# Kernel tuning notes

Hardware: AMD Instinct MI355X
Metric: run time of the kernel (lower is better)

The kernel has to match this reference:

```python
import jax, jax.numpy as jnp
import numpy as np

N = 100000   # entities
T = 4        # edge types
E = 250000   # edges per type
D = 64       # dimension
H = 4        # attention heads
C = 64       # per-head out channels (PyG out_channels)
F_IN = 256   # raw feature dim
L = 2        # num_layers
NEG_SLOPE = 0.2


def setup_inputs() -> dict:
    key = jax.random.key(0)
    ks = jax.random.split(key, 10)
    return {
        "feature_matrix": jax.random.normal(ks[0], (N, F_IN), jnp.float32),
        "entity_emb": jax.random.normal(ks[1], (N + 1, D), jnp.float32),
        "lin_w": jax.random.normal(ks[2], (F_IN, D), jnp.float32) * 0.05,
        "lin_b": jnp.zeros((D,), jnp.float32),
        "ln_g": jnp.ones((D,), jnp.float32),
        "ln_b": jnp.zeros((D,), jnp.float32),
        "W_src": jax.random.normal(ks[3], (L, T, D, H * C), jnp.float32) * 0.1,
        "W_dst": jax.random.normal(ks[4], (L, T, D, H * C), jnp.float32) * 0.1,
        "a_src": jax.random.normal(ks[5], (L, T, H, C), jnp.float32) * 0.1,
        "a_dst": jax.random.normal(ks[6], (L, T, H, C), jnp.float32) * 0.1,
        "conv_bias": jnp.zeros((L, T, C), jnp.float32),
        "edge_index": jax.random.randint(ks[7], (T, 2, E), 0, N, jnp.int32),
    }


def _layer_norm(x, g, b):
    mu = jnp.mean(x, axis=-1, keepdims=True)
    var = jnp.var(x, axis=-1, keepdims=True)
    return (x - mu) * jax.lax.rsqrt(var + 1e-5) * g + b


def _l2_normalize(x):
    n = jnp.linalg.norm(x, axis=-1, keepdims=True)
    return x / jnp.maximum(n, 1e-12)


def _gat_conv(x, src, dst, Ws, Wd, a_s, a_d, bias):
    # x: [N, D]; src/dst: [E'] (self loops already appended, PyG default)
    xs = (x @ Ws).reshape(N, H, C)          # source projection per head
    xd = (x @ Wd).reshape(N, H, C)          # destination projection per head
    logit = (xs * a_s).sum(-1)[src] + (xd * a_d).sum(-1)[dst]  # [E', H]
    logit = jax.nn.leaky_relu(logit, NEG_SLOPE)
    # segment softmax over incoming edges of each dst node
    m = jax.lax.stop_gradient(jax.ops.segment_max(logit, dst, num_segments=N))
    p = jnp.exp(logit - m[dst])
    s = jax.ops.segment_sum(p, dst, num_segments=N)
    alpha = p / s[dst]                       # [E', H]
    msg = xs[src] * alpha[..., None]         # [E', H, C]
    out = jax.ops.segment_sum(msg.reshape(-1, H * C), dst, num_segments=N)
    out = out.reshape(N, H, C).mean(axis=1)  # concat=False -> head mean
    return out + bias


def reference(feature_matrix, entity_emb, lin_w, lin_b, ln_g, ln_b,
              W_src, W_dst, a_src, a_dst, conv_bias, edge_index):
    # feature_transform: Linear -> LayerNorm -> GELU (exact erf GELU, torch default)
    xf = jax.nn.gelu(_layer_norm(feature_matrix @ lin_w + lin_b, ln_g, ln_b),
                     approximate=False)
    xe = _l2_normalize(entity_emb[:N])
    x = xf + xe
    loop = jnp.arange(N, dtype=edge_index.dtype)
    for l in range(L):
        acc = jnp.zeros((N, C), x.dtype)
        for t in range(T):
            src = jnp.concatenate([edge_index[t, 0], loop])
            dst = jnp.concatenate([edge_index[t, 1], loop])
            acc = acc + _gat_conv(x, src, dst, W_src[l, t], W_dst[l, t],
                                  a_src[l, t], a_dst[l, t], conv_bias[l, t])
        x = jax.nn.gelu(acc / T, approximate=False)  # HeteroConv aggr='mean'; dropout=eval identity
    return x
```

## Files before the change

kernel.cpp:

```cpp
#include <hip/hip_runtime.h>
#include <hip/hip_bf16.h>
#include <cstdint>

#define NN   100000
#define TT   4
#define EE   250000
#define LL   2
#define NCH  49
#define EPN  (EE + NN)
#define N64  ((size_t)NN * 64)

typedef unsigned short ushort_t;
typedef __attribute__((ext_vector_type(8))) short bf16x8;
typedef __attribute__((ext_vector_type(16))) float floatx16;

static __device__ __forceinline__ float gelu_exact(float v) {
    return 0.5f * v * (1.0f + erff(v * 0.7071067811865476f));
}
static __device__ __forceinline__ float wave_sum64(float v) {
    #pragma unroll
    for (int m = 32; m; m >>= 1) v += __shfl_xor(v, m, 64);
    return v;
}
static __device__ __forceinline__ ushort_t f2bf(float f) {
    unsigned u = __float_as_uint(f);
    u += 0x7FFFu + ((u >> 16) & 1u);
    return (ushort_t)(u >> 16);
}
static __device__ __forceinline__ float bf2f(ushort_t h) {
    return __uint_as_float((unsigned)h << 16);
}

__global__ __launch_bounds__(256) void k_prep(
    const float* __restrict__ Wsrc, const float* __restrict__ Wdst,
    const float* __restrict__ asrc, const float* __restrict__ adst,
    const float* __restrict__ cb, const float* __restrict__ lin_w,
    ushort_t* __restrict__ wcTh, ushort_t* __restrict__ wcTl,
    ushort_t* __restrict__ lwTh, ushort_t* __restrict__ lwTl,
    ushort_t* __restrict__ bpTh, ushort_t* __restrict__ bpTl,
    float* __restrict__ bsum)
{
    int id = blockIdx.x * 256 + threadIdx.x;
    {
        int d = id & 63;
        int c = (id >> 6) & 63;
        int h = (id >> 12) & 3;
        int t = (id >> 14) & 3;
        int l = (id >> 16) & 1;
        float v = 0.25f * Wsrc[(((l * 4 + t) * 64 + d) * 256) + h * 64 + c];
        int dst = (l * 64 + c) * 1024 + (t * 256 + h * 64 + d);
        ushort_t hh = f2bf(v);
        bpTh[dst] = hh;
        bpTl[dst] = f2bf(v - bf2f(hh));
    }
    if (id < LL * 64 * 64) {
        int d   = id & 63;
        int col = (id >> 6) & 63;
        int l   = (id >> 12) & 1;
        int t = col >> 3, side = (col >> 2) & 1, h = col & 3;
        const float* W = side ? Wdst : Wsrc;
        const float* a = side ? adst : asrc;
        int wb = ((l * 4 + t) * 64 + d) * 256 + h * 64;
        int ab = ((l * 4 + t) * 4 + h) * 64;
        float s = 0.f;
        #pragma unroll 8
        for (int c2 = 0; c2 < 64; ++c2) s = fmaf(W[wb + c2], a[ab + c2], s);
        int dst = (l * 64 + col) * 64 + d;
        ushort_t hh = f2bf(s);
        wcTh[dst] = hh;
        wcTl[dst] = f2bf(s - bf2f(hh));
    }
    if (id < 64 * 256) {
        int k = id & 255, c = id >> 8;
        float v = lin_w[k * 64 + c];
        ushort_t hh = f2bf(v);
        lwTh[c * 256 + k] = hh;
        lwTl[c * 256 + k] = f2bf(v - bf2f(hh));
    }
    if (id < LL * 64) {
        int l = id >> 6, c = id & 63;
        float s = 0.f;
        for (int t = 0; t < TT; ++t) s += cb[(l * 4 + t) * 64 + c];
        bsum[id] = s;
    }
}

__global__ void k_hist(const int* __restrict__ ei, int* __restrict__ cursor) {
    int id = blockIdx.x * 256 + threadIdx.x;
    if (id >= TT * EE) return;
    int t = id / EE, e = id - t * EE;
    int d = ei[(t * 2 + 1) * EE + e];
    atomicAdd(&cursor[t * NN + d], 1);
}

__global__ __launch_bounds__(256) void k_scan1(const int* __restrict__ deg,
                                               int* __restrict__ csum) {
    int b = blockIdx.x, t = b / NCH, cc = b - t * NCH;
    int tid = threadIdx.x;
    int base = cc * 2048 + tid * 8;
    int s = 0;
    #pragma unroll
    for (int i = 0; i < 8; ++i) {
        int idx = base + i;
        if (idx < NN) s += deg[t * NN + idx] + 1;
    }
    #pragma unroll
    for (int m = 32; m; m >>= 1) s += __shfl_xor(s, m, 64);
    __shared__ int ws4[4];
    int lane = tid & 63, wid = tid >> 6;
    if (lane == 0) ws4[wid] = s;
    __syncthreads();
    if (tid == 0) csum[b] = ws4[0] + ws4[1] + ws4[2] + ws4[3];
}

__global__ void k_scan2(const int* __restrict__ csum, int* __restrict__ cbase,
                        int* __restrict__ row_ptr) {
    int t = threadIdx.x;
    if (t >= TT) return;
    int base = 0;
    for (int c = 0; c < NCH; ++c) {
        cbase[t * NCH + c] = base;
        base += csum[t * NCH + c];
    }
    row_ptr[t * (NN + 1) + NN] = base;
}

__global__ __launch_bounds__(256) void k_scan3(int* __restrict__ cursor,
                                               const int* __restrict__ cbase,
                                               int* __restrict__ row_ptr) {
    int b = blockIdx.x, t = b / NCH, cc = b - t * NCH;
    int tid = threadIdx.x, lane = tid & 63, wid = tid >> 6;
    int base = cc * 2048 + tid * 8;
    int vals[8], ts = 0;
    #pragma unroll
    for (int i = 0; i < 8; ++i) {
        int idx = base + i;
        int v = (idx < NN) ? cursor[t * NN + idx] + 1 : 0;
        vals[i] = v; ts += v;
    }
    int v = ts;
    #pragma unroll
    for (int off = 1; off < 64; off <<= 1) {
        int u = __shfl_up(v, off, 64);
        if (lane >= off) v += u;
    }
    __shared__ int wt[4];
    if (lane == 63) wt[wid] = v;
    __syncthreads();
    int wbase = 0;
    for (int w = 0; w < wid; ++w) wbase += wt[w];
    int run = cbase[t * NCH + cc] + wbase + (v - ts);
    #pragma unroll
    for (int i = 0; i < 8; ++i) {
        int idx = base + i;
        if (idx < NN) {
            row_ptr[t * (NN + 1) + idx] = run;
            cursor[t * NN + idx] = run;
        }
        run += vals[i];
    }
}

__global__ void k_scatter(const int* __restrict__ ei, int* __restrict__ cursor,
                          int* __restrict__ col) {
    int id = blockIdx.x * 256 + threadIdx.x;
    if (id >= TT * EPN) return;
    int t = id / EPN, r = id - t * EPN;
    int s, d;
    if (r < EE) { s = ei[t * 2 * EE + r]; d = ei[(t * 2 + 1) * EE + r]; }
    else        { s = d = r - EE; }
    int pos = atomicAdd(&cursor[t * NN + d], 1);
    col[(size_t)t * EPN + pos] = s;
}

__global__ void k_split(const float* __restrict__ in, ushort_t* __restrict__ hi,
                        ushort_t* __restrict__ lo, int n4) {
    int i = blockIdx.x * 256 + threadIdx.x;
    if (i >= n4) return;
    float4 v = ((const float4*)in)[i];
    ushort_t h0 = f2bf(v.x), h1 = f2bf(v.y), h2 = f2bf(v.z), h3 = f2bf(v.w);
    ushort4 hv = make_ushort4(h0, h1, h2, h3);
    ushort4 lv = make_ushort4(f2bf(v.x - bf2f(h0)), f2bf(v.y - bf2f(h1)),
                              f2bf(v.z - bf2f(h2)), f2bf(v.w - bf2f(h3)));
    ((ushort4*)hi)[i] = hv;
    ((ushort4*)lo)[i] = lv;
}

template <int FLAGS>
__global__ __launch_bounds__(256, 4) void k_gemm_mx(
    const ushort_t* __restrict__ Ahi, const ushort_t* __restrict__ Alo,
    const ushort_t* __restrict__ Bhi, const ushort_t* __restrict__ Blo,
    int K, int ldb, int nrows,
    const float* __restrict__ accbuf, const float* __restrict__ bias,
    float* __restrict__ Cout, ushort_t* __restrict__ Chi, ushort_t* __restrict__ Clo)
{
    constexpr int KC = 32, LK = 40;
    __shared__ ushort_t sAh[128 * LK], sAl[128 * LK];
    __shared__ ushort_t sBh[64 * LK],  sBl[64 * LK];
    const int tid = threadIdx.x;
    const int w = tid >> 6, ln = tid & 63;
    const int l31 = ln & 31, hl = ln >> 5;
    const int rowbase = blockIdx.x * 128;

    floatx16 accv[2];
    #pragma unroll
    for (int ct = 0; ct < 2; ++ct)
        #pragma unroll
        for (int r = 0; r < 16; ++r) accv[ct][r] = 0.f;

    for (int kc = 0; kc < K; kc += KC) {
        __syncthreads();
        #pragma unroll
        for (int i = 0; i < 2; ++i) {
            int f = tid + i * 256;
            int r = f >> 2, cg = f & 3;
            int row = rowbase + r;
            int so = r * LK + cg * 8;
            if (row < nrows) {
                size_t ga = (size_t)row * K + kc + cg * 8;
                *(uint4*)&sAh[so] = *(const uint4*)(Ahi + ga);
                *(uint4*)&sAl[so] = *(const uint4*)(Alo + ga);
            } else {
                *(uint4*)&sAh[so] = make_uint4(0, 0, 0, 0);
                *(uint4*)&sAl[so] = make_uint4(0, 0, 0, 0);
            }
        }
        {
            int r = tid >> 2, cg = tid & 3;
            size_t gb = (size_t)r * ldb + kc + cg * 8;
            int so = r * LK + cg * 8;
            *(uint4*)&sBh[so] = *(const uint4*)(Bhi + gb);
            *(uint4*)&sBl[so] = *(const uint4*)(Blo + gb);
        }
        __syncthreads();
        const int arow = (w << 5) + l31;
        #pragma unroll
        for (int s = 0; s < 2; ++s) {
            const int koff = (s << 4) + (hl << 3);
            bf16x8 ah  = *(const bf16x8*)&sAh[arow * LK + koff];
            bf16x8 al  = *(const bf16x8*)&sAl[arow * LK + koff];
            bf16x8 bh0 = *(const bf16x8*)&sBh[l31 * LK + koff];
            bf16x8 bl0 = *(const bf16x8*)&sBl[l31 * LK + koff];
            bf16x8 bh1 = *(const bf16x8*)&sBh[(32 + l31) * LK + koff];
            bf16x8 bl1 = *(const bf16x8*)&sBl[(32 + l31) * LK + koff];
            accv[0] = __builtin_amdgcn_mfma_f32_32x32x16_bf16(ah, bh0, accv[0], 0, 0, 0);
            accv[1] = __builtin_amdgcn_mfma_f32_32x32x16_bf16(ah, bh1, accv[1], 0, 0, 0);
            accv[0] = __builtin_amdgcn_mfma_f32_32x32x16_bf16(al, bh0, accv[0], 0, 0, 0);
            accv[1] = __builtin_amdgcn_mfma_f32_32x32x16_bf16(al, bh1, accv[1], 0, 0, 0);
            accv[0] = __builtin_amdgcn_mfma_f32_32x32x16_bf16(ah, bl0, accv[0], 0, 0, 0);
            accv[1] = __builtin_amdgcn_mfma_f32_32x32x16_bf16(ah, bl1, accv[1], 0, 0, 0);
        }
    }
    #pragma unroll
    for (int ct = 0; ct < 2; ++ct) {
        int col = (ct << 5) + l31;
        float bv = (FLAGS & 2) ? bias[col] : 0.f;
        #pragma unroll
        for (int r = 0; r < 16; ++r) {
            int row = rowbase + (w << 5) + (r & 3) + ((r >> 2) << 3) + (hl << 2);
            if (row < nrows) {
                size_t idx = (size_t)row * 64 + col;
                float v = accv[ct][r];
                if (FLAGS & 1) v += accbuf[idx];
                if (FLAGS & 2) v = gelu_exact((v + bv) * 0.25f);
                Cout[idx] = v;
                if (FLAGS & 4) {
                    ushort_t hh = f2bf(v);
                    Chi[idx] = hh;
                    Clo[idx] = f2bf(v - bf2f(hh));
                }
            }
        }
    }
}

__global__ __launch_bounds__(256) void k_feat_post(
    const float* __restrict__ y, const float* __restrict__ lin_b,
    const float* __restrict__ ln_g, const float* __restrict__ ln_b,
    const float* __restrict__ emb, float* __restrict__ xout,
    ushort_t* __restrict__ xh, ushort_t* __restrict__ xl)
{
    int n = (blockIdx.x << 2) + (threadIdx.x >> 6);
    int c = threadIdx.x & 63;
    size_t base = (size_t)n * 64 + c;
    float v = y[base] + lin_b[c];
    float mean = wave_sum64(v) * 0.015625f;
    float t = v - mean;
    float var = wave_sum64(t * t) * 0.015625f;
    float vn = t * (1.0f / sqrtf(var + 1e-5f)) * ln_g[c] + ln_b[c];
    float g = gelu_exact(vn);
    float e = emb[base];
    float nrm = sqrtf(wave_sum64(e * e));
    float xv = g + e / fmaxf(nrm, 1e-12f);
    xout[base] = xv;
    ushort_t hh = f2bf(xv);
    xh[base] = hh;
    xl[base] = f2bf(xv - bf2f(hh));
}

__global__ __launch_bounds__(256) void k_edge2(
    const float* __restrict__ x, const float* __restrict__ s_all,
    const int* __restrict__ row_ptr, const int* __restrict__ col,
    ushort_t* __restrict__ zh, ushort_t* __restrict__ zl, int t0, int nt)
{
    int n = (blockIdx.x << 2) + (threadIdx.x >> 6);
    int lane = threadIdx.x & 63;
    int zrow = nt * 256;
    for (int tt = 0; tt < nt; ++tt) {
        int t = t0 + tt;
        int rp0 = row_ptr[t * (NN + 1) + n];
        int rp1 = row_ptr[t * (NN + 1) + n + 1];
        const int* colt = col + (size_t)t * EPN;
        const float4 sd = *(const float4*)&s_all[(size_t)n * 64 + t * 8 + 4];
        float z0 = 0.f, z1 = 0.f, z2 = 0.f, z3 = 0.f;
        float S0 = 0.f, S1 = 0.f, S2 = 0.f, S3 = 0.f;
        #pragma unroll 2
        for (int e = rp0; e < rp1; ++e) {
            int s = colt[e];
            const float4 ss = *(const float4*)&s_all[(size_t)s * 64 + t * 8];
            float l0 = ss.x + sd.x, l1 = ss.y + sd.y;
            float l2 = ss.z + sd.z, l3 = ss.w + sd.w;
            l0 = l0 > 0.f ? l0 : 0.2f * l0;
            l1 = l1 > 0.f ? l1 : 0.2f * l1;
            l2 = l2 > 0.f ? l2 : 0.2f * l2;
            l3 = l3 > 0.f ? l3 : 0.2f * l3;
            float p0 = __expf(l0), p1 = __expf(l1);
            float p2 = __expf(l2), p3 = __expf(l3);
            S0 += p0; S1 += p1; S2 += p2; S3 += p3;
            float xv = x[(size_t)s * 64 + lane];
            z0 = fmaf(p0, xv, z0);
            z1 = fmaf(p1, xv, z1);
            z2 = fmaf(p2, xv, z2);
            z3 = fmaf(p3, xv, z3);
        }
        size_t zb = (size_t)n * zrow + tt * 256 + lane;
        float v0 = z0 / S0, v1 = z1 / S1, v2 = z2 / S2, v3 = z3 / S3;
        ushort_t h0 = f2bf(v0), h1 = f2bf(v1), h2 = f2bf(v2), h3 = f2bf(v3);
        zh[zb]       = h0;  zl[zb]       = f2bf(v0 - bf2f(h0));
        zh[zb + 64]  = h1;  zl[zb + 64]  = f2bf(v1 - bf2f(h1));
        zh[zb + 128] = h2;  zl[zb + 128] = f2bf(v2 - bf2f(h2));
        zh[zb + 192] = h3;  zl[zb + 192] = f2bf(v3 - bf2f(h3));
    }
}

extern "C" void kernel_launch(void* const* d_in, const int* in_sizes, int n_in,
                              void* d_out, int out_size, void* d_ws, size_t ws_size,
                              hipStream_t stream) {
    const float* fm    = (const float*)d_in[0];
    const float* emb   = (const float*)d_in[1];
    const float* lin_w = (const float*)d_in[2];
    const float* lin_b = (const float*)d_in[3];
    const float* ln_g  = (const float*)d_in[4];
    const float* ln_b  = (const float*)d_in[5];
    const float* Wsrc  = (const float*)d_in[6];
    const float* Wdst  = (const float*)d_in[7];
    const float* asrc  = (const float*)d_in[8];
    const float* adst  = (const float*)d_in[9];
    const float* cbias = (const float*)d_in[10];
    const int*   ei    = (const int*)d_in[11];
    float* out = (float*)d_out;
    (void)in_sizes; (void)n_in; (void)out_size;

    char* w = (char*)d_ws;
    size_t off = 0;
    auto alloc = [&](size_t bytes) -> void* {
        void* p = w + off;
        off += (bytes + 255) & ~(size_t)255;
        return p;
    };
    ushort_t* wcTh = (ushort_t*)alloc((size_t)LL * 64 * 64 * 2);
    ushort_t* wcTl = (ushort_t*)alloc((size_t)LL * 64 * 64 * 2);
    ushort_t* lwTh = (ushort_t*)alloc((size_t)64 * 256 * 2);
    ushort_t* lwTl = (ushort_t*)alloc((size_t)64 * 256 * 2);
    ushort_t* bpTh = (ushort_t*)alloc((size_t)LL * 64 * 1024 * 2);
    ushort_t* bpTl = (ushort_t*)alloc((size_t)LL * 64 * 1024 * 2);
    float* bsum    = (float*)alloc((size_t)LL * 64 * 4);
    int*   row_ptr = (int*)  alloc((size_t)TT * (NN + 1) * 4);
    int*   cursor  = (int*)  alloc((size_t)TT * NN * 4);
    int*   colarr  = (int*)  alloc((size_t)TT * EPN * 4);
    int*   csum    = (int*)  alloc((size_t)TT * NCH * 4);
    int*   cbase   = (int*)  alloc((size_t)TT * NCH * 4);
    float* x       = (float*)alloc(N64 * 4);
    ushort_t* xh   = (ushort_t*)alloc(N64 * 2);
    ushort_t* xl   = (ushort_t*)alloc(N64 * 2);
    float* s_all   = (float*)alloc(N64 * 4);
    float* accB    = (float*)alloc(N64 * 4);
    size_t rem = (ws_size > off) ? (ws_size - off) : 0;
    int NT = 1;
    if (rem >= (size_t)NN * 1024 * 4 + (8u << 20)) NT = 4;
    else if (rem >= (size_t)NN * 512 * 4 + (8u << 20)) NT = 2;
    size_t planeE = (size_t)NN * 256 * NT;
    char* big = (char*)alloc(2 * planeE * 2 < 2 * (size_t)NN * 256 * 2
                             ? 2 * (size_t)NN * 256 * 2 : 2 * planeE * 2);
    ushort_t* fmh = (ushort_t*)big;
    ushort_t* fml = fmh + (size_t)NN * 256;
    ushort_t* zh  = (ushort_t*)big;
    ushort_t* zl  = zh + planeE;

    hipMemsetAsync(cursor, 0, (size_t)TT * NN * 4, stream);
    k_prep<<<512, 256, 0, stream>>>(Wsrc, Wdst, asrc, adst, cbias, lin_w,
                                    wcTh, wcTl, lwTh, lwTl, bpTh, bpTl, bsum);
    k_hist<<<(TT * EE + 255) / 256, 256, 0, stream>>>(ei, cursor);
    k_scan1<<<TT * NCH, 256, 0, stream>>>(cursor, csum);
    k_scan2<<<1, 64, 0, stream>>>(csum, cbase, row_ptr);
    k_scan3<<<TT * NCH, 256, 0, stream>>>(cursor, cbase, row_ptr);
    k_scatter<<<(TT * EPN + 255) / 256, 256, 0, stream>>>(ei, cursor, colarr);

    const int GB = (NN + 127) / 128;
    k_split<<<(NN * 64 + 255) / 256, 256, 0, stream>>>(fm, fmh, fml, NN * 64);
    k_gemm_mx<0><<<GB, 256, 0, stream>>>(fmh, fml, lwTh, lwTl, 256, 256, NN,
                                         nullptr, nullptr, accB, nullptr, nullptr);
    k_feat_post<<<NN / 4, 256, 0, stream>>>(accB, lin_b, ln_g, ln_b, emb, x, xh, xl);

    const int nb = TT / NT;
    for (int l = 0; l < LL; ++l) {
        k_gemm_mx<0><<<GB, 256, 0, stream>>>(xh, xl, wcTh + l * 4096, wcTl + l * 4096,
                                             64, 64, NN, nullptr, nullptr,
                                             s_all, nullptr, nullptr);
        float* dest = (l == 0) ? x : out;
        const ushort_t* Bh = bpTh + (size_t)l * 65536;
        const ushort_t* Bl = bpTl + (size_t)l * 65536;
        for (int b = 0; b < nb; ++b) {
            k_edge2<<<NN / 4, 256, 0, stream>>>(x, s_all, row_ptr, colarr,
                                                zh, zl, b * NT, NT);
            int K = NT * 256;
            const ushort_t* Bhb = Bh + b * K;
            const ushort_t* Blb = Bl + b * K;
            bool last = (b == nb - 1);
            if (!last) {
                if (b == 0)
                    k_gemm_mx<0><<<GB, 256, 0, stream>>>(zh, zl, Bhb, Blb, K, 1024, NN,
                                                         nullptr, nullptr, accB,
                                                         nullptr, nullptr);
                else
                    k_gemm_mx<1><<<GB, 256, 0, stream>>>(zh, zl, Bhb, Blb, K, 1024, NN,
                                                         accB, nullptr, accB,
                                                         nullptr, nullptr);
            } else {
                if (nb == 1) {
                    if (l == 0)
                        k_gemm_mx<6><<<GB, 256, 0, stream>>>(zh, zl, Bhb, Blb, K, 1024,
                                                             NN, nullptr, bsum + l * 64,
                                                             dest, xh, xl);
                    else
                        k_gemm_mx<2><<<GB, 256, 0, stream>>>(zh, zl, Bhb, Blb, K, 1024,
                                                             NN, nullptr, bsum + l * 64,
                                                             dest, nullptr, nullptr);
                } else {
                    if (l == 0)
                        k_gemm_mx<7><<<GB, 256, 0, stream>>>(zh, zl, Bhb, Blb, K, 1024,
                                                             NN, accB, bsum + l * 64,
                                                             dest, xh, xl);
                    else
                        k_gemm_mx<3><<<GB, 256, 0, stream>>>(zh, zl, Bhb, Blb, K, 1024,
                                                             NN, accB, bsum + l * 64,
                                                             dest, nullptr, nullptr);
                }
            }
        }
    }
}
```

Measured before the change: 1.057 ms.

## Fuse bf16 split into GEMM loads and precompute per-edge attention weights

The GEMM gains a mode that loads fp32 A tiles and splits them into bf16 hi/lo pairs in registers. This removes the separate k_split pass and the hi/lo copies of x written by feat_post and the layer-0 epilogue. Attention exponentials are now computed once per edge in a new k_edgep kernel, with coalesced edge-parallel reads, and stored in a buffer that k_edge2 reads. That takes the leaky-relu and exp work off the gather loop, at the cost of extra memory traffic for a per-edge dst array and a 4-float-per-edge weight buffer.

```diff
diff --git a/kernel.cpp b/kernel.cpp
--- a/kernel.cpp
+++ b/kernel.cpp
@@ -162,7 +162,7 @@
 }
 
 __global__ void k_scatter(const int* __restrict__ ei, int* __restrict__ cursor,
-                          int* __restrict__ col) {
+                          int* __restrict__ col, int* __restrict__ dstarr) {
     int id = blockIdx.x * 256 + threadIdx.x;
     if (id >= TT * EPN) return;
     int t = id / EPN, r = id - t * EPN;
@@ -171,19 +171,7 @@
     else        { s = d = r - EE; }
     int pos = atomicAdd(&cursor[t * NN + d], 1);
     col[(size_t)t * EPN + pos] = s;
-}
-
-__global__ void k_split(const float* __restrict__ in, ushort_t* __restrict__ hi,
-                        ushort_t* __restrict__ lo, int n4) {
-    int i = blockIdx.x * 256 + threadIdx.x;
-    if (i >= n4) return;
-    float4 v = ((const float4*)in)[i];
-    ushort_t h0 = f2bf(v.x), h1 = f2bf(v.y), h2 = f2bf(v.z), h3 = f2bf(v.w);
-    ushort4 hv = make_ushort4(h0, h1, h2, h3);
-    ushort4 lv = make_ushort4(f2bf(v.x - bf2f(h0)), f2bf(v.y - bf2f(h1)),
-                              f2bf(v.z - bf2f(h2)), f2bf(v.w - bf2f(h3)));
-    ((ushort4*)hi)[i] = hv;
-    ((ushort4*)lo)[i] = lv;
+    dstarr[(size_t)t * EPN + pos] = d;
 }
 
 template <int FLAGS>
@@ -218,8 +206,28 @@
             int so = r * LK + cg * 8;
             if (row < nrows) {
                 size_t ga = (size_t)row * K + kc + cg * 8;
-                *(uint4*)&sAh[so] = *(const uint4*)(Ahi + ga);
-                *(uint4*)&sAl[so] = *(const uint4*)(Alo + ga);
+                if constexpr (FLAGS & 8) {
+                    const float* Af = (const float*)Ahi;
+                    float4 v0 = *(const float4*)(Af + ga);
+                    float4 v1 = *(const float4*)(Af + ga + 4);
+                    float vf[8] = {v0.x, v0.y, v0.z, v0.w, v1.x, v1.y, v1.z, v1.w};
+                    unsigned hu[8], lu[8];
+                    #pragma unroll
+                    for (int q = 0; q < 8; ++q) {
+                        ushort_t hh = f2bf(vf[q]);
+                        hu[q] = hh;
+                        lu[q] = f2bf(vf[q] - bf2f(hh));
+                    }
+                    uint4 H = make_uint4(hu[0] | (hu[1] << 16), hu[2] | (hu[3] << 16),
+                                         hu[4] | (hu[5] << 16), hu[6] | (hu[7] << 16));
+                    uint4 L = make_uint4(lu[0] | (lu[1] << 16), lu[2] | (lu[3] << 16),
+                                         lu[4] | (lu[5] << 16), lu[6] | (lu[7] << 16));
+                    *(uint4*)&sAh[so] = H;
+                    *(uint4*)&sAl[so] = L;
+                } else {
+                    *(uint4*)&sAh[so] = *(const uint4*)(Ahi + ga);
+                    *(uint4*)&sAl[so] = *(const uint4*)(Alo + ga);
+                }
             } else {
                 *(uint4*)&sAh[so] = make_uint4(0, 0, 0, 0);
                 *(uint4*)&sAl[so] = make_uint4(0, 0, 0, 0);
@@ -277,8 +285,7 @@
 __global__ __launch_bounds__(256) void k_feat_post(
     const float* __restrict__ y, const float* __restrict__ lin_b,
     const float* __restrict__ ln_g, const float* __restrict__ ln_b,
-    const float* __restrict__ emb, float* __restrict__ xout,
-    ushort_t* __restrict__ xh, ushort_t* __restrict__ xl)
+    const float* __restrict__ emb, float* __restrict__ xout)
 {
     int n = (blockIdx.x << 2) + (threadIdx.x >> 6);
     int c = threadIdx.x & 63;
@@ -293,13 +300,31 @@
     float nrm = sqrtf(wave_sum64(e * e));
     float xv = g + e / fmaxf(nrm, 1e-12f);
     xout[base] = xv;
-    ushort_t hh = f2bf(xv);
-    xh[base] = hh;
-    xl[base] = f2bf(xv - bf2f(hh));
+}
+
+__global__ __launch_bounds__(256) void k_edgep(
+    const float* __restrict__ s_all, const int* __restrict__ col,
+    const int* __restrict__ dstarr, float* __restrict__ parr)
+{
+    int i = blockIdx.x * 256 + threadIdx.x;
+    int t = blockIdx.y;
+    if (i >= EPN) return;
+    size_t base = (size_t)t * EPN + i;
+    int s = col[base], d = dstarr[base];
+    const float4 a = *(const float4*)&s_all[(size_t)s * 64 + t * 8];
+    const float4 b = *(const float4*)&s_all[(size_t)d * 64 + t * 8 + 4];
+    float l0 = a.x + b.x, l1 = a.y + b.y;
+    float l2 = a.z + b.z, l3 = a.w + b.w;
+    l0 = l0 > 0.f ? l0 : 0.2f * l0;
+    l1 = l1 > 0.f ? l1 : 0.2f * l1;
+    l2 = l2 > 0.f ? l2 : 0.2f * l2;
+    l3 = l3 > 0.f ? l3 : 0.2f * l3;
+    float4 p = make_float4(__expf(l0), __expf(l1), __expf(l2), __expf(l3));
+    *(float4*)&parr[base * 4] = p;
 }
 
 __global__ __launch_bounds__(256) void k_edge2(
-    const float* __restrict__ x, const float* __restrict__ s_all,
+    const float* __restrict__ x, const float* __restrict__ parr,
     const int* __restrict__ row_ptr, const int* __restrict__ col,
     ushort_t* __restrict__ zh, ushort_t* __restrict__ zl, int t0, int nt)
 {
@@ -311,27 +336,19 @@
         int rp0 = row_ptr[t * (NN + 1) + n];
         int rp1 = row_ptr[t * (NN + 1) + n + 1];
         const int* colt = col + (size_t)t * EPN;
-        const float4 sd = *(const float4*)&s_all[(size_t)n * 64 + t * 8 + 4];
+        const float4* pt = (const float4*)parr + (size_t)t * EPN;
         float z0 = 0.f, z1 = 0.f, z2 = 0.f, z3 = 0.f;
         float S0 = 0.f, S1 = 0.f, S2 = 0.f, S3 = 0.f;
         #pragma unroll 2
         for (int e = rp0; e < rp1; ++e) {
             int s = colt[e];
-            const float4 ss = *(const float4*)&s_all[(size_t)s * 64 + t * 8];
-            float l0 = ss.x + sd.x, l1 = ss.y + sd.y;
-            float l2 = ss.z + sd.z, l3 = ss.w + sd.w;
-            l0 = l0 > 0.f ? l0 : 0.2f * l0;
-            l1 = l1 > 0.f ? l1 : 0.2f * l1;
-            l2 = l2 > 0.f ? l2 : 0.2f * l2;
-            l3 = l3 > 0.f ? l3 : 0.2f * l3;
-            float p0 = __expf(l0), p1 = __expf(l1);
-            float p2 = __expf(l2), p3 = __expf(l3);
-            S0 += p0; S1 += p1; S2 += p2; S3 += p3;
+            float4 p = pt[e];
             float xv = x[(size_t)s * 64 + lane];
-            z0 = fmaf(p0, xv, z0);
-            z1 = fmaf(p1, xv, z1);
-            z2 = fmaf(p2, xv, z2);
-            z3 = fmaf(p3, xv, z3);
+            S0 += p.x; S1 += p.y; S2 += p.z; S3 += p.w;
+            z0 = fmaf(p.x, xv, z0);
+            z1 = fmaf(p.y, xv, z1);
+            z2 = fmaf(p.z, xv, z2);
+            z3 = fmaf(p.w, xv, z3);
         }
         size_t zb = (size_t)n * zrow + tt * 256 + lane;
         float v0 = z0 / S0, v1 = z1 / S1, v2 = z2 / S2, v3 = z3 / S3;
@@ -378,11 +395,11 @@
     int*   row_ptr = (int*)  alloc((size_t)TT * (NN + 1) * 4);
     int*   cursor  = (int*)  alloc((size_t)TT * NN * 4);
     int*   colarr  = (int*)  alloc((size_t)TT * EPN * 4);
+    int*   dstarr  = (int*)  alloc((size_t)TT * EPN * 4);
+    float* parr    = (float*)alloc((size_t)TT * EPN * 4 * 4);
     int*   csum    = (int*)  alloc((size_t)TT * NCH * 4);
     int*   cbase   = (int*)  alloc((size_t)TT * NCH * 4);
     float* x       = (float*)alloc(N64 * 4);
-    ushort_t* xh   = (ushort_t*)alloc(N64 * 2);
-    ushort_t* xl   = (ushort_t*)alloc(N64 * 2);
     float* s_all   = (float*)alloc(N64 * 4);
     float* accB    = (float*)alloc(N64 * 4);
     size_t rem = (ws_size > off) ? (ws_size - off) : 0;
@@ -390,12 +407,8 @@
     if (rem >= (size_t)NN * 1024 * 4 + (8u << 20)) NT = 4;
     else if (rem >= (size_t)NN * 512 * 4 + (8u << 20)) NT = 2;
     size_t planeE = (size_t)NN * 256 * NT;
-    char* big = (char*)alloc(2 * planeE * 2 < 2 * (size_t)NN * 256 * 2
-                             ? 2 * (size_t)NN * 256 * 2 : 2 * planeE * 2);
-    ushort_t* fmh = (ushort_t*)big;
-    ushort_t* fml = fmh + (size_t)NN * 256;
-    ushort_t* zh  = (ushort_t*)big;
-    ushort_t* zl  = zh + planeE;
+    ushort_t* zh = (ushort_t*)alloc(2 * planeE * 2);
+    ushort_t* zl = zh + planeE;
 
     hipMemsetAsync(cursor, 0, (size_t)TT * NN * 4, stream);
     k_prep<<<512, 256, 0, stream>>>(Wsrc, Wdst, asrc, adst, cbias, lin_w,
@@ -404,24 +417,27 @@
     k_scan1<<<TT * NCH, 256, 0, stream>>>(cursor, csum);
     k_scan2<<<1, 64, 0, stream>>>(csum, cbase, row_ptr);
     k_scan3<<<TT * NCH, 256, 0, stream>>>(cursor, cbase, row_ptr);
-    k_scatter<<<(TT * EPN + 255) / 256, 256, 0, stream>>>(ei, cursor, colarr);
+    k_scatter<<<(TT * EPN + 255) / 256, 256, 0, stream>>>(ei, cursor, colarr, dstarr);
 
     const int GB = (NN + 127) / 128;
-    k_split<<<(NN * 64 + 255) / 256, 256, 0, stream>>>(fm, fmh, fml, NN * 64);
-    k_gemm_mx<0><<<GB, 256, 0, stream>>>(fmh, fml, lwTh, lwTl, 256, 256, NN,
+    k_gemm_mx<8><<<GB, 256, 0, stream>>>((const ushort_t*)fm, nullptr,
+                                         lwTh, lwTl, 256, 256, NN,
                                          nullptr, nullptr, accB, nullptr, nullptr);
-    k_feat_post<<<NN / 4, 256, 0, stream>>>(accB, lin_b, ln_g, ln_b, emb, x, xh, xl);
+    k_feat_post<<<NN / 4, 256, 0, stream>>>(accB, lin_b, ln_g, ln_b, emb, x);
 
     const int nb = TT / NT;
+    const dim3 gp((EPN + 255) / 256, TT);
     for (int l = 0; l < LL; ++l) {
-        k_gemm_mx<0><<<GB, 256, 0, stream>>>(xh, xl, wcTh + l * 4096, wcTl + l * 4096,
+        k_gemm_mx<8><<<GB, 256, 0, stream>>>((const ushort_t*)x, nullptr,
+                                             wcTh + l * 4096, wcTl + l * 4096,
                                              64, 64, NN, nullptr, nullptr,
                                              s_all, nullptr, nullptr);
+        k_edgep<<<gp, 256, 0, stream>>>(s_all, colarr, dstarr, parr);
         float* dest = (l == 0) ? x : out;
         const ushort_t* Bh = bpTh + (size_t)l * 65536;
         const ushort_t* Bl = bpTl + (size_t)l * 65536;
         for (int b = 0; b < nb; ++b) {
-            k_edge2<<<NN / 4, 256, 0, stream>>>(x, s_all, row_ptr, colarr,
+            k_edge2<<<NN / 4, 256, 0, stream>>>(x, parr, row_ptr, colarr,
                                                 zh, zl, b * NT, NT);
             int K = NT * 256;
             const ushort_t* Bhb = Bh + b * K;
@@ -437,25 +453,14 @@
                                                          accB, nullptr, accB,
                                                          nullptr, nullptr);
             } else {
-                if (nb == 1) {
-                    if (l == 0)
-                        k_gemm_mx<6><<<GB, 256, 0, stream>>>(zh, zl, Bhb, Blb, K, 1024,
-                                                             NN, nullptr, bsum + l * 64,
-                                                             dest, xh, xl);
-                    else
-                        k_gemm_mx<2><<<GB, 256, 0, stream>>>(zh, zl, Bhb, Blb, K, 1024,
-                                                             NN, nullptr, bsum + l * 64,
-                                                             dest, nullptr, nullptr);
-                } else {
-                    if (l == 0)
-                        k_gemm_mx<7><<<GB, 256, 0, stream>>>(zh, zl, Bhb, Blb, K, 1024,
-                                                             NN, accB, bsum + l * 64,
-                                                             dest, xh, xl);
-                    else
-                        k_gemm_mx<3><<<GB, 256, 0, stream>>>(zh, zl, Bhb, Blb, K, 1024,
-                                                             NN, accB, bsum + l * 64,
-                                                             dest, nullptr, nullptr);
-                }
+                if (nb == 1)
+                    k_gemm_mx<2><<<GB, 256, 0, stream>>>(zh, zl, Bhb, Blb, K, 1024,
+                                                         NN, nullptr, bsum + l * 64,
+                                                         dest, nullptr, nullptr);
+                else
+                    k_gemm_mx<3><<<GB, 256, 0, stream>>>(zh, zl, Bhb, Blb, K, 1024,
+                                                         NN, accB, bsum + l * 64,
+                                                         dest, nullptr, nullptr);
             }
         }
     }
```

After: 1.042 ms. Within noise of the previous version (-1.5%).
